# Performance work log

Measured on AMD Instinct MI355X. Metric: run time of the kernel, lower is better.

Reference implementation:

```python
import jax, jax.numpy as jnp
import numpy as np

B, D, HGT, WID = 32, 512, 8, 32   # batch, channels, feature map H, W
T = HGT * WID                     # 256 spatial tokens
NH, L, MAXLEN = 8, 2, 25          # heads, encoder layers, max text len


def _ln(x, s, b, eps=1e-5):
    m = jnp.mean(x, -1, keepdims=True)
    v = jnp.mean((x - m) ** 2, -1, keepdims=True)
    return (x - m) * jax.lax.rsqrt(v + eps) * s + b


def setup_inputs() -> dict:
    key = jax.random.key(0)
    ks = jax.random.split(key, 16)
    w = lambda k, shp: jax.random.normal(k, shp, jnp.float32) * 0.02
    return {
        "x": jax.random.normal(ks[0], (B, D, HGT, WID), jnp.float32),
        "encoder_word_pos": jnp.arange(T, dtype=jnp.int32),
        "gsrm_word_pos": jnp.arange(MAXLEN, dtype=jnp.int32),
        # encoder positional table
        "pos_table": w(ks[1], (T, D)),
        # per-layer encoder params (stacked over L)
        "ln1_s": jnp.ones((L, D), jnp.float32), "ln1_b": jnp.zeros((L, D), jnp.float32),
        "Wq": w(ks[2], (L, D, D)), "bq": jnp.zeros((L, D), jnp.float32),
        "Wk": w(ks[3], (L, D, D)), "bk": jnp.zeros((L, D), jnp.float32),
        "Wv": w(ks[4], (L, D, D)), "bv": jnp.zeros((L, D), jnp.float32),
        "Wo": w(ks[5], (L, D, D)), "bo": jnp.zeros((L, D), jnp.float32),
        "ln2_s": jnp.ones((L, D), jnp.float32), "ln2_b": jnp.zeros((L, D), jnp.float32),
        "W1": w(ks[6], (L, D, D)), "b1": jnp.zeros((L, D), jnp.float32),  # d_inner_hid = hidden_dim
        "W2": w(ks[7], (L, D, D)), "b2": jnp.zeros((L, D), jnp.float32),
        "lnf_s": jnp.ones((D,), jnp.float32), "lnf_b": jnp.zeros((D,), jnp.float32),
        # PVAM head params
        "fc0_w": w(ks[8], (D, D)), "fc0_b": jnp.zeros((D,), jnp.float32),
        "emb_table": w(ks[9], (MAXLEN, D)),
        "fc1_w": w(ks[10], (D,)),
    }


def _pvam(x, encoder_word_pos, gsrm_word_pos, pos_table,
          ln1_s, ln1_b, Wq, bq, Wk, bk, Wv, bv, Wo, bo,
          ln2_s, ln2_b, W1, b1, W2, b2, lnf_s, lnf_b,
          fc0_w, fc0_b, emb_table, fc1_w):
    b, c, h, wd = x.shape
    feat = x.reshape(b, c, h * wd).transpose(0, 2, 1)          # [b, t, c]
    # prepare encoder: scale + learned positional embedding (eval mode: no dropout)
    enc = feat * jnp.sqrt(jnp.float32(c)) + pos_table[encoder_word_pos]
    dk = c // NH
    scale = 1.0 / jnp.sqrt(jnp.float32(dk))
    for l in range(L):  # pre-norm transformer encoder (preprocess='n', postprocess='da')
        qin = _ln(enc, ln1_s[l], ln1_b[l])
        q = (qin @ Wq[l] + bq[l]).reshape(b, -1, NH, dk)
        k = (qin @ Wk[l] + bk[l]).reshape(b, -1, NH, dk)
        v = (qin @ Wv[l] + bv[l]).reshape(b, -1, NH, dk)
        p = jax.nn.softmax(jnp.einsum('bqhd,bkhd->bhqk', q, k) * scale, -1)
        o = jnp.einsum('bhqk,bkhd->bqhd', p, v).reshape(b, -1, c)
        enc = enc + (o @ Wo[l] + bo[l])
        y = _ln(enc, ln2_s[l], ln2_b[l])
        enc = enc + (jax.nn.relu(y @ W1[l] + b1[l]) @ W2[l] + b2[l])
    enc = _ln(enc, lnf_s, lnf_b)
    word_features = enc @ fc0_w + fc0_b                        # [b, t, c]
    word_pos = emb_table[gsrm_word_pos]                        # [max_len, c]
    # additive attention: tanh(broadcast add) -> scalar score -> softmax over t
    y = jnp.tanh(word_features[:, None, :, :] + word_pos[None, :, None, :])  # [b,max_len,t,c]
    attn = jax.nn.softmax(jnp.einsum('bmtc,c->bmt', y, fc1_w), -1)
    return jnp.einsum('bmt,btc->bmc', attn, word_features)    # [b, max_len, c]


def reference(x, encoder_word_pos, gsrm_word_pos, pos_table,
              ln1_s, ln1_b, Wq, bq, Wk, bk, Wv, bv, Wo, bo,
              ln2_s, ln2_b, W1, b1, W2, b2, lnf_s, lnf_b,
              fc0_w, fc0_b, emb_table, fc1_w):
    return _pvam(x, encoder_word_pos, gsrm_word_pos, pos_table,
                 ln1_s, ln1_b, Wq, bq, Wk, bk, Wv, bv, Wo, bo,
                 ln2_s, ln2_b, W1, b1, W2, b2, lnf_s, lnf_b,
                 fc0_w, fc0_b, emb_table, fc1_w)
```

## Files before the change

### kernel.cpp

```cpp
#include <hip/hip_runtime.h>
#include <math.h>

#define B_ 32
#define D_ 512
#define T_ 256
#define NH_ 8
#define DK_ 64
#define ML_ 25

typedef unsigned short ushort_t;
using short8 = __attribute__((ext_vector_type(8))) short;
using f32x4  = __attribute__((ext_vector_type(4))) float;

__device__ __forceinline__ ushort_t f2bf(float f) {
    unsigned u = __float_as_uint(f);
    unsigned r = (u + 0x7fffu + ((u >> 16) & 1u)) >> 16;
    return (ushort_t)r;
}
__device__ __forceinline__ float bf2f(ushort_t h) {
    return __uint_as_float(((unsigned)h) << 16);
}
__device__ __forceinline__ void gl16(const void* g, void* l) {
    __builtin_amdgcn_global_load_lds((const __attribute__((address_space(1))) void*)g,
                                     (__attribute__((address_space(3))) void*)l, 16, 0, 0);
}
#define ZERO4(v) { (v)[0]=0.f; (v)[1]=0.f; (v)[2]=0.f; (v)[3]=0.f; }

__global__ __launch_bounds__(256) void prep_kernel(const float* __restrict__ x,
                                                   const int* __restrict__ epos,
                                                   const float* __restrict__ pos,
                                                   float* __restrict__ enc) {
    __shared__ float ld[64][65];
    int tt = blockIdx.x, ct = blockIdx.y, b = blockIdx.z;
    int t0 = tt * 64, c0 = ct * 64;
    int tid = threadIdx.x;
    int r = tid >> 4, c4 = (tid & 15) << 2;
#pragma unroll
    for (int p = 0; p < 4; p++) {
        int row = p * 16 + r;
        float4 v = *(const float4*)(x + ((size_t)(b * D_ + c0 + row) * T_ + t0) + c4);
        ld[row][c4 + 0] = v.x; ld[row][c4 + 1] = v.y; ld[row][c4 + 2] = v.z; ld[row][c4 + 3] = v.w;
    }
    __syncthreads();
#pragma unroll
    for (int p = 0; p < 4; p++) {
        int tr = p * 16 + r;
        int ep = epos[t0 + tr];
        float4 pv = *(const float4*)(pos + (size_t)ep * D_ + c0 + c4);
        float4 o;
        o.x = ld[c4 + 0][tr] * 22.627417f + pv.x;
        o.y = ld[c4 + 1][tr] * 22.627417f + pv.y;
        o.z = ld[c4 + 2][tr] * 22.627417f + pv.z;
        o.w = ld[c4 + 3][tr] * 22.627417f + pv.w;
        *(float4*)(enc + (size_t)(b * T_ + t0 + tr) * D_ + c0 + c4) = o;
    }
}

__global__ __launch_bounds__(256) void convert_w_kernel(const float* __restrict__ Wq,
                                                        const float* __restrict__ Wk,
                                                        const float* __restrict__ Wv,
                                                        const float* __restrict__ Wo,
                                                        const float* __restrict__ W1,
                                                        const float* __restrict__ W2,
                                                        const float* __restrict__ fc0,
                                                        ushort_t* __restrict__ wt) {
    __shared__ float ld[64][65];
    int m = blockIdx.x >> 6;
    int tile = blockIdx.x & 63;
    int tn = tile >> 3, tk = tile & 7;
    int n0 = tn * 64, k0 = tk * 64;
    const float* src;
    if (m < 12) {
        int l = m / 6, w = m % 6;
        const float* bases[6] = {Wq, Wk, Wv, Wo, W1, W2};
        src = bases[w] + (size_t)l * D_ * D_;
    } else {
        src = fc0;
    }
    int tid = threadIdx.x;
    int r = tid >> 4, c4 = (tid & 15) << 2;
#pragma unroll
    for (int p = 0; p < 4; p++) {
        int row = p * 16 + r;
        float4 v = *(const float4*)(src + (size_t)(k0 + row) * D_ + n0 + c4);
        ld[row][c4 + 0] = v.x; ld[row][c4 + 1] = v.y; ld[row][c4 + 2] = v.z; ld[row][c4 + 3] = v.w;
    }
    __syncthreads();
    ushort_t* dsth = wt + (size_t)m * D_ * D_;
    ushort_t* dstl = wt + (size_t)13 * D_ * D_;
#pragma unroll
    for (int p = 0; p < 4; p++) {
        int n = p * 16 + r;
        int kc = c4;
        ushort_t h[4], lo[4];
#pragma unroll
        for (int i = 0; i < 4; i++) {
            float f = ld[kc + i][n];
            h[i] = f2bf(f);
            lo[i] = f2bf(f - bf2f(h[i]));
        }
        *(ushort4*)(dsth + (size_t)(n0 + n) * D_ + k0 + kc) = make_ushort4(h[0], h[1], h[2], h[3]);
        if (m == 12)
            *(ushort4*)(dstl + (size_t)(n0 + n) * D_ + k0 + kc) = make_ushort4(lo[0], lo[1], lo[2], lo[3]);
    }
}

template<bool LO>
__global__ __launch_bounds__(256) void ln_kernel(const float* __restrict__ x,
                                                 const float* __restrict__ s,
                                                 const float* __restrict__ b,
                                                 ushort_t* __restrict__ yh,
                                                 ushort_t* __restrict__ yl) {
    int wid = threadIdx.x >> 6, lane = threadIdx.x & 63;
    size_t row = (size_t)blockIdx.x * 4 + wid;
    const float4* xr = (const float4*)(x + row * D_);
    float4 v0 = xr[lane * 2], v1 = xr[lane * 2 + 1];
    float sum = v0.x + v0.y + v0.z + v0.w + v1.x + v1.y + v1.z + v1.w;
    for (int o = 32; o; o >>= 1) sum += __shfl_xor(sum, o);
    float mean = sum * (1.f / 512.f);
    float d[8] = {v0.x - mean, v0.y - mean, v0.z - mean, v0.w - mean,
                  v1.x - mean, v1.y - mean, v1.z - mean, v1.w - mean};
    float vs = 0.f;
#pragma unroll
    for (int i = 0; i < 8; i++) vs += d[i] * d[i];
    for (int o = 32; o; o >>= 1) vs += __shfl_xor(vs, o);
    float rs = 1.f / sqrtf(vs * (1.f / 512.f) + 1e-5f);
    const float4* s4 = (const float4*)s;
    const float4* b4 = (const float4*)b;
    float4 sa = s4[lane * 2], sb = s4[lane * 2 + 1];
    float4 ba = b4[lane * 2], bb = b4[lane * 2 + 1];
    float o8[8];
    o8[0] = d[0] * rs * sa.x + ba.x; o8[1] = d[1] * rs * sa.y + ba.y;
    o8[2] = d[2] * rs * sa.z + ba.z; o8[3] = d[3] * rs * sa.w + ba.w;
    o8[4] = d[4] * rs * sb.x + bb.x; o8[5] = d[5] * rs * sb.y + bb.y;
    o8[6] = d[6] * rs * sb.z + bb.z; o8[7] = d[7] * rs * sb.w + bb.w;
    ushort_t h[8];
#pragma unroll
    for (int i = 0; i < 8; i++) h[i] = f2bf(o8[i]);
    uint4 u;
    u.x = (unsigned)h[0] | ((unsigned)h[1] << 16);
    u.y = (unsigned)h[2] | ((unsigned)h[3] << 16);
    u.z = (unsigned)h[4] | ((unsigned)h[5] << 16);
    u.w = (unsigned)h[6] | ((unsigned)h[7] << 16);
    *(uint4*)(yh + row * D_ + lane * 8) = u;
    if (LO) {
        ushort_t l8[8];
#pragma unroll
        for (int i = 0; i < 8; i++) l8[i] = f2bf(o8[i] - bf2f(h[i]));
        uint4 ul;
        ul.x = (unsigned)l8[0] | ((unsigned)l8[1] << 16);
        ul.y = (unsigned)l8[2] | ((unsigned)l8[3] << 16);
        ul.z = (unsigned)l8[4] | ((unsigned)l8[5] << 16);
        ul.w = (unsigned)l8[6] | ((unsigned)l8[7] << 16);
        *(uint4*)(yl + row * D_ + lane * 8) = ul;
    }
}

template<int EPI>
__global__ __launch_bounds__(256) void gemm_kernel(const ushort_t* __restrict__ A0,
                                                   const ushort_t* __restrict__ A1,
                                                   const ushort_t* __restrict__ A2,
                                                   const ushort_t* __restrict__ B0,
                                                   const ushort_t* __restrict__ B1,
                                                   const ushort_t* __restrict__ B2,
                                                   int nseg, int nbn,
                                                   const float* __restrict__ bias,
                                                   const float* __restrict__ bias2,
                                                   const float* __restrict__ bias3,
                                                   const float* __restrict__ res,
                                                   float* __restrict__ outF,
                                                   ushort_t* __restrict__ outB) {
    __shared__ ushort_t As[2][128 * 64];
    __shared__ ushort_t Bs[2][128 * 64];
    int tid = threadIdx.x;
    int g = blockIdx.x;
    int per = gridDim.x >> 3;
    int lin = (g & 7) * per + (g >> 3);
    int bm = lin / nbn, bn = lin % nbn;

    int lane = tid & 63;
    int wid = tid >> 6;
    int wm = wid >> 1, wn = wid & 1;
    int xr = (lane & 7) << 3;

    f32x4 acc[4][4];
#pragma unroll
    for (int i = 0; i < 4; i++)
#pragma unroll
        for (int j = 0; j < 4; j++) ZERO4(acc[i][j]);

    int nt = nseg * 8;

#define STAGE(kt, buf)                                                                  \
    {                                                                                   \
        int seg_ = (kt) >> 3;                                                           \
        int k0_ = ((kt) & 7) * 64;                                                      \
        const ushort_t* Asg = seg_ == 0 ? A0 : (seg_ == 1 ? A1 : A2);                   \
        const ushort_t* Bsg = seg_ == 0 ? B0 : (seg_ == 1 ? B1 : B2);                   \
        _Pragma("unroll")                                                               \
        for (int it = 0; it < 4; it++) {                                                \
            int uu = tid + it * 256;                                                    \
            int row_ = uu >> 3;                                                         \
            int kb_ = (((uu & 7) ^ (row_ & 7)) << 3);                                   \
            gl16(Asg + (size_t)(bm * 128 + row_) * 512 + k0_ + kb_, &As[buf][uu * 8]);  \
            gl16(Bsg + (size_t)(bn * 128 + row_) * 512 + k0_ + kb_, &Bs[buf][uu * 8]);  \
        }                                                                               \
    }

    STAGE(0, 0);
    asm volatile("s_waitcnt vmcnt(0)" ::: "memory");
    __syncthreads();

    int buf = 0;
    for (int t = 0; t < nt; t++) {
        if (t + 1 < nt) STAGE(t + 1, buf ^ 1);
#pragma unroll
        for (int kc = 0; kc < 2; kc++) {
            short8 a[4], b[4];
            int koff = (kc * 32 + ((lane >> 4) << 3)) ^ xr;
#pragma unroll
            for (int i = 0; i < 4; i++)
                a[i] = *(const short8*)&As[buf][(wm * 64 + i * 16 + (lane & 15)) * 64 + koff];
#pragma unroll
            for (int j = 0; j < 4; j++)
                b[j] = *(const short8*)&Bs[buf][(wn * 64 + j * 16 + (lane & 15)) * 64 + koff];
#pragma unroll
            for (int i = 0; i < 4; i++)
#pragma unroll
                for (int j = 0; j < 4; j++)
                    acc[i][j] = __builtin_amdgcn_mfma_f32_16x16x32_bf16(a[i], b[j], acc[i][j], 0, 0, 0);
        }
        asm volatile("s_waitcnt vmcnt(0)" ::: "memory");
        __syncthreads();
        buf ^= 1;
    }
#undef STAGE

#pragma unroll
    for (int i = 0; i < 4; i++) {
#pragma unroll
        for (int j = 0; j < 4; j++) {
            int r0 = bm * 128 + wm * 64 + i * 16 + ((lane >> 4) << 2);
            int col = bn * 128 + wn * 64 + j * 16 + (lane & 15);
            int seg = col >> 9;
            int ccol = col & 511;
            const float* bp = bias;
            if (EPI == 5) bp = (seg == 0) ? bias : (seg == 1 ? bias2 : bias3);
            float bc = bp[EPI == 5 ? ccol : col];
#pragma unroll
            for (int jj = 0; jj < 4; jj++) {
                float v = acc[i][j][jj] + bc;
                int row = r0 + jj;
                size_t idx = (size_t)row * 512 + col;
                if (EPI == 2) {
                    outF[idx] = v + res[idx];
                } else if (EPI == 3) {
                    outB[idx] = f2bf(fmaxf(v, 0.f));
                } else if (EPI == 4) {
                    outF[idx] = v;
                } else if (EPI == 5) {
                    if (seg < 2) {
                        outB[(size_t)seg * 4194304 + (size_t)row * 512 + ccol] = f2bf(v);
                    } else {
                        int bb2 = row >> 8, t2 = row & 255;
                        outB[(size_t)2 * 4194304 +
                             ((size_t)(bb2 * 8 + (ccol >> 6)) * 64 + (ccol & 63)) * 256 + t2] = f2bf(v);
                    }
                }
            }
        }
    }
}

__global__ __launch_bounds__(256) void attn_fused_kernel(const ushort_t* __restrict__ q,
                                                         const ushort_t* __restrict__ k,
                                                         const ushort_t* __restrict__ vt,
                                                         ushort_t* __restrict__ ao) {
    __shared__ ushort_t KVs[256 * 64];
    __shared__ ushort_t Ps[64 * 256];
    int tid = threadIdx.x;
    int lane = tid & 63;
    int wid = tid >> 6;
    int m0 = blockIdx.x * 64;
    int bh = blockIdx.y;
    int b = bh >> 3, h = bh & 7;
    int xr = (lane & 7) << 3;

#pragma unroll
    for (int it = 0; it < 8; it++) {
        int uu = tid + it * 256;
        int row = uu >> 3;
        int gx = ((uu & 7) ^ (row & 7)) << 3;
        gl16(k + (size_t)(b * T_ + row) * D_ + h * DK_ + gx, &KVs[uu * 8]);
    }
    short8 qa0, qa1;
    {
        int qrow = m0 + wid * 16 + (lane & 15);
        const ushort_t* qp = q + (size_t)(b * T_ + qrow) * D_ + h * DK_ + ((lane >> 4) << 3);
        qa0 = *(const short8*)(qp);
        qa1 = *(const short8*)(qp + 32);
    }
    f32x4 acc[16];
#pragma unroll
    for (int j = 0; j < 16; j++) ZERO4(acc[j]);
    asm volatile("s_waitcnt vmcnt(0)" ::: "memory");
    __syncthreads();

#pragma unroll
    for (int j = 0; j < 16; j++) {
        int krow = j * 16 + (lane & 15);
        short8 b0 = *(const short8*)&KVs[krow * 64 + ((((lane >> 4) << 3)) ^ xr)];
        short8 b1 = *(const short8*)&KVs[krow * 64 + ((32 + ((lane >> 4) << 3)) ^ xr)];
        acc[j] = __builtin_amdgcn_mfma_f32_16x16x32_bf16(qa0, b0, acc[j], 0, 0, 0);
        acc[j] = __builtin_amdgcn_mfma_f32_16x16x32_bf16(qa1, b1, acc[j], 0, 0, 0);
    }
    __syncthreads();

#pragma unroll
    for (int it = 0; it < 8; it++) {
        int uu = tid + it * 256;
        int row = uu >> 5;
        int gx = ((uu & 31) ^ (row & 7)) << 3;
        gl16(vt + ((size_t)bh * DK_ + row) * T_ + gx, &KVs[uu * 8]);
    }

    const float C = 0.125f * 1.44269504f;
#pragma unroll
    for (int jj = 0; jj < 4; jj++) {
        float mx = -1e30f;
#pragma unroll
        for (int j = 0; j < 16; j++) mx = fmaxf(mx, acc[j][jj]);
#pragma unroll
        for (int msk = 1; msk < 16; msk <<= 1) mx = fmaxf(mx, __shfl_xor(mx, msk));
        float sm = 0.f;
#pragma unroll
        for (int j = 0; j < 16; j++) {
            float e = __builtin_amdgcn_exp2f((acc[j][jj] - mx) * C);
            acc[j][jj] = e;
            sm += e;
        }
#pragma unroll
        for (int msk = 1; msk < 16; msk <<= 1) sm += __shfl_xor(sm, msk);
        float inv = 1.f / sm;
#pragma unroll
        for (int j = 0; j < 16; j++) acc[j][jj] *= inv;
    }
#pragma unroll
    for (int j = 0; j < 16; j++) {
#pragma unroll
        for (int jj = 0; jj < 4; jj++) {
            int row = wid * 16 + ((lane >> 4) << 2) + jj;
            int col = j * 16 + (lane & 15);
            Ps[row * 256 + (col ^ ((row & 7) << 3))] = f2bf(acc[j][jj]);
        }
    }
    asm volatile("s_waitcnt vmcnt(0)" ::: "memory");
    __syncthreads();

    int wm = wid >> 1, wn = wid & 1;
    f32x4 acc2[2][2];
#pragma unroll
    for (int i = 0; i < 2; i++)
#pragma unroll
        for (int j = 0; j < 2; j++) ZERO4(acc2[i][j]);
#pragma unroll
    for (int kc = 0; kc < 8; kc++) {
        int off = (kc * 32 + ((lane >> 4) << 3)) ^ xr;
        short8 a0 = *(const short8*)&Ps[(wm * 32 + (lane & 15)) * 256 + off];
        short8 a1 = *(const short8*)&Ps[(wm * 32 + 16 + (lane & 15)) * 256 + off];
        short8 b0 = *(const short8*)&KVs[(wn * 32 + (lane & 15)) * 256 + off];
        short8 b1 = *(const short8*)&KVs[(wn * 32 + 16 + (lane & 15)) * 256 + off];
        acc2[0][0] = __builtin_amdgcn_mfma_f32_16x16x32_bf16(a0, b0, acc2[0][0], 0, 0, 0);
        acc2[0][1] = __builtin_amdgcn_mfma_f32_16x16x32_bf16(a0, b1, acc2[0][1], 0, 0, 0);
        acc2[1][0] = __builtin_amdgcn_mfma_f32_16x16x32_bf16(a1, b0, acc2[1][0], 0, 0, 0);
        acc2[1][1] = __builtin_amdgcn_mfma_f32_16x16x32_bf16(a1, b1, acc2[1][1], 0, 0, 0);
    }
#pragma unroll
    for (int i = 0; i < 2; i++)
#pragma unroll
        for (int j = 0; j < 2; j++)
#pragma unroll
            for (int jj = 0; jj < 4; jj++)
                ao[(size_t)(b * T_ + m0 + wm * 32 + i * 16 + ((lane >> 4) << 2) + jj) * D_ +
                   h * DK_ + wn * 32 + j * 16 + (lane & 15)] = f2bf(acc2[i][j][jj]);
}

__global__ __launch_bounds__(256) void scores_kernel(const float* __restrict__ wf,
                                                     const int* __restrict__ gpos,
                                                     const float* __restrict__ emb,
                                                     const float* __restrict__ w1,
                                                     float* __restrict__ scores) {
    __shared__ float wpL[5][512];
    __shared__ float w1m2[512];
    const float K2 = 2.885390082f;
    int tid = threadIdx.x;
    int b = blockIdx.y;
    int mg = blockIdx.z * 5;
    int t = blockIdx.x * 32 + (tid >> 3);
    int cg = tid & 7;
    for (int idx = tid; idx < 5 * 128; idx += 256) {
        int m = idx >> 7, w4 = idx & 127;
        float4 v = *(const float4*)(emb + (size_t)gpos[mg + m] * D_ + (w4 << 2));
        v.x *= K2; v.y *= K2; v.z *= K2; v.w *= K2;
        *(float4*)&wpL[m][w4 << 2] = v;
    }
    if (tid < 128) {
        float4 v = *(const float4*)(w1 + (tid << 2));
        v.x *= -2.f; v.y *= -2.f; v.z *= -2.f; v.w *= -2.f;
        *(float4*)&w1m2[tid << 2] = v;
    }
    float4 wfs[16];
    float W1S = 0.f;
    const float* wfr = wf + (size_t)(b * T_ + t) * D_ + (cg << 2);
#pragma unroll
    for (int j = 0; j < 16; j++) {
        float4 v = *(const float4*)(wfr + (j << 5));
        wfs[j].x = v.x * K2; wfs[j].y = v.y * K2; wfs[j].z = v.z * K2; wfs[j].w = v.w * K2;
        float4 wv = *(const float4*)(w1 + (cg << 2) + (j << 5));
        W1S += wv.x + wv.y + wv.z + wv.w;
    }
    __syncthreads();
    float s[5] = {W1S, W1S, W1S, W1S, W1S};
#pragma unroll
    for (int j = 0; j < 16; j++) {
        float4 w14 = *(const float4*)&w1m2[(cg << 2) + (j << 5)];
#pragma unroll
        for (int m = 0; m < 5; m++) {
            float4 wp4 = *(const float4*)&wpL[m][(cg << 2) + (j << 5)];
            s[m] += w14.x * __builtin_amdgcn_rcpf(__builtin_amdgcn_exp2f(wfs[j].x + wp4.x) + 1.f);
            s[m] += w14.y * __builtin_amdgcn_rcpf(__builtin_amdgcn_exp2f(wfs[j].y + wp4.y) + 1.f);
            s[m] += w14.z * __builtin_amdgcn_rcpf(__builtin_amdgcn_exp2f(wfs[j].z + wp4.z) + 1.f);
            s[m] += w14.w * __builtin_amdgcn_rcpf(__builtin_amdgcn_exp2f(wfs[j].w + wp4.w) + 1.f);
        }
    }
#pragma unroll
    for (int m = 0; m < 5; m++) {
        s[m] += __shfl_xor(s[m], 1);
        s[m] += __shfl_xor(s[m], 2);
        s[m] += __shfl_xor(s[m], 4);
    }
    if (cg == 0) {
#pragma unroll
        for (int m = 0; m < 5; m++)
            scores[((size_t)b * ML_ + mg + m) * T_ + t] = s[m];
    }
}

__global__ __launch_bounds__(256) void softmax_kernel(float* __restrict__ sc) {
    int wid = threadIdx.x >> 6, lane = threadIdx.x & 63;
    size_t row = (size_t)blockIdx.x * 4 + wid;
    float4* p = (float4*)(sc + row * T_);
    float4 v = p[lane];
    float mx = fmaxf(fmaxf(v.x, v.y), fmaxf(v.z, v.w));
    for (int o = 32; o; o >>= 1) mx = fmaxf(mx, __shfl_xor(mx, o));
    float4 e;
    e.x = __expf(v.x - mx); e.y = __expf(v.y - mx);
    e.z = __expf(v.z - mx); e.w = __expf(v.w - mx);
    float sm = e.x + e.y + e.z + e.w;
    for (int o = 32; o; o >>= 1) sm += __shfl_xor(sm, o);
    float inv = 1.f / sm;
    e.x *= inv; e.y *= inv; e.z *= inv; e.w *= inv;
    p[lane] = e;
}

__global__ __launch_bounds__(256) void wsum_kernel(const float* __restrict__ attn,
                                                   const float* __restrict__ wf,
                                                   float* __restrict__ out) {
    __shared__ float at[T_][8];
    int tid = threadIdx.x;
    int b = blockIdx.y, m0 = blockIdx.x * 5;
#pragma unroll
    for (int q = 0; q < 5; q++) {
        float a = attn[((size_t)b * ML_ + m0 + q) * T_ + tid];
        at[tid][q] = a;
    }
    __syncthreads();
    int c0 = tid << 1;
    const float* wfb = wf + (size_t)b * T_ * D_ + c0;
    float acc[5][2] = {};
    for (int t = 0; t < T_; t++) {
        float2 v = *(const float2*)(wfb + (size_t)t * D_);
        float4 a4 = *(const float4*)&at[t][0];
        float a5 = at[t][4];
        acc[0][0] += a4.x * v.x; acc[0][1] += a4.x * v.y;
        acc[1][0] += a4.y * v.x; acc[1][1] += a4.y * v.y;
        acc[2][0] += a4.z * v.x; acc[2][1] += a4.z * v.y;
        acc[3][0] += a4.w * v.x; acc[3][1] += a4.w * v.y;
        acc[4][0] += a5 * v.x;   acc[4][1] += a5 * v.y;
    }
#pragma unroll
    for (int q = 0; q < 5; q++) {
        float2 o;
        o.x = acc[q][0]; o.y = acc[q][1];
        *(float2*)(out + ((size_t)b * ML_ + m0 + q) * D_ + c0) = o;
    }
}

extern "C" void kernel_launch(void* const* d_in, const int* in_sizes, int n_in,
                              void* d_out, int out_size, void* d_ws, size_t ws_size,
                              hipStream_t stream) {
    (void)in_sizes; (void)n_in; (void)out_size; (void)ws_size;
    const float* x        = (const float*)d_in[0];
    const int*   epos     = (const int*)d_in[1];
    const int*   gpos     = (const int*)d_in[2];
    const float* pos_tab  = (const float*)d_in[3];
    const float* ln1_s    = (const float*)d_in[4];
    const float* ln1_b    = (const float*)d_in[5];
    const float* Wq       = (const float*)d_in[6];
    const float* bq       = (const float*)d_in[7];
    const float* Wk       = (const float*)d_in[8];
    const float* bk       = (const float*)d_in[9];
    const float* Wv       = (const float*)d_in[10];
    const float* bv       = (const float*)d_in[11];
    const float* Wo       = (const float*)d_in[12];
    const float* bo       = (const float*)d_in[13];
    const float* ln2_s    = (const float*)d_in[14];
    const float* ln2_b    = (const float*)d_in[15];
    const float* W1       = (const float*)d_in[16];
    const float* b1       = (const float*)d_in[17];
    const float* W2       = (const float*)d_in[18];
    const float* b2       = (const float*)d_in[19];
    const float* lnf_s    = (const float*)d_in[20];
    const float* lnf_b    = (const float*)d_in[21];
    const float* fc0_w    = (const float*)d_in[22];
    const float* fc0_b    = (const float*)d_in[23];
    const float* emb      = (const float*)d_in[24];
    const float* fc1_w    = (const float*)d_in[25];

    char* ws = (char*)d_ws;
    float*    enc = (float*)(ws);
    ushort_t* hi  = (ushort_t*)(ws + 16777216);
    ushort_t* qb  = (ushort_t*)(ws + 25165824);
    ushort_t* kb  = (ushort_t*)(ws + 33554432);
    ushort_t* lo  = (ushort_t*)(ws + 33554432);
    float*    scb = (float*)(ws + 33554432);
    ushort_t* vt  = (ushort_t*)(ws + 41943040);
    ushort_t* h1  = (ushort_t*)(ws + 41943040);
    ushort_t* ao  = (ushort_t*)(ws + 50331648);
    float*    wf  = (float*)(ws + 58720256);
    ushort_t* wt  = (ushort_t*)(ws + 75497472);
    const size_t WSL = (size_t)D_ * D_;

    convert_w_kernel<<<13 * 64, 256, 0, stream>>>(Wq, Wk, Wv, Wo, W1, W2, fc0_w, wt);
    prep_kernel<<<dim3(4, 8, 32), 256, 0, stream>>>(x, epos, pos_tab, enc);

    for (int l = 0; l < 2; l++) {
        size_t o1 = (size_t)l * D_;
        const ushort_t* WqkvT = wt + (l * 6 + 0) * WSL;
        const ushort_t* WoT = wt + (l * 6 + 3) * WSL;
        const ushort_t* W1T = wt + (l * 6 + 4) * WSL;
        const ushort_t* W2T = wt + (l * 6 + 5) * WSL;

        ln_kernel<false><<<2048, 256, 0, stream>>>(enc, ln1_s + o1, ln1_b + o1, hi, nullptr);
        gemm_kernel<5><<<768, 256, 0, stream>>>(hi, nullptr, nullptr, WqkvT, nullptr, nullptr,
                                                1, 12, bq + o1, bk + o1, bv + o1, nullptr, nullptr, qb);
        attn_fused_kernel<<<dim3(4, 256), 256, 0, stream>>>(qb, kb, vt, ao);
        gemm_kernel<2><<<256, 256, 0, stream>>>(ao, nullptr, nullptr, WoT, nullptr, nullptr,
                                                1, 4, bo + o1, nullptr, nullptr, enc, enc, nullptr);
        ln_kernel<false><<<2048, 256, 0, stream>>>(enc, ln2_s + o1, ln2_b + o1, hi, nullptr);
        gemm_kernel<3><<<256, 256, 0, stream>>>(hi, nullptr, nullptr, W1T, nullptr, nullptr,
                                                1, 4, b1 + o1, nullptr, nullptr, nullptr, nullptr, h1);
        gemm_kernel<2><<<256, 256, 0, stream>>>(h1, nullptr, nullptr, W2T, nullptr, nullptr,
                                                1, 4, b2 + o1, nullptr, nullptr, enc, enc, nullptr);
    }

    ln_kernel<true><<<2048, 256, 0, stream>>>(enc, lnf_s, lnf_b, hi, lo);
    gemm_kernel<4><<<256, 256, 0, stream>>>(hi, lo, hi, wt + 12 * WSL, wt + 12 * WSL, wt + 13 * WSL,
                                            3, 4, fc0_b, nullptr, nullptr, nullptr, wf, nullptr);
    scores_kernel<<<dim3(8, 32, 5), 256, 0, stream>>>(wf, gpos, emb, fc1_w, scb);
    softmax_kernel<<<200, 256, 0, stream>>>(scb);
    wsum_kernel<<<dim3(5, 32), 256, 0, stream>>>(scb, wf, (float*)d_out);
}
```

Baseline: 309.9 us.

## Narrow GEMM N-tile to 64 and deepen LDS pipeline to three stages

The GEMM tile shrinks from 128x128 to 128x64, which doubles the grid for every GEMM launch so more CUs are busy for these small M=8192 problems. LDS staging moves from double to triple buffering, and a partial vmcnt wait lets loads for two future k-tiles stay in flight while the current one is computed. In exchange, each block reuses its A tile less, so A traffic grows, and the MFMA work per LDS read drops.

```diff
diff --git a/kernel.cpp b/kernel.cpp
--- a/kernel.cpp
+++ b/kernel.cpp
@@ -170,8 +170,8 @@
                                                    const float* __restrict__ res,
                                                    float* __restrict__ outF,
                                                    ushort_t* __restrict__ outB) {
-    __shared__ ushort_t As[2][128 * 64];
-    __shared__ ushort_t Bs[2][128 * 64];
+    __shared__ ushort_t As[3][128 * 64];
+    __shared__ ushort_t Bs[3][64 * 64];
     int tid = threadIdx.x;
     int g = blockIdx.x;
     int per = gridDim.x >> 3;
@@ -183,11 +183,11 @@
     int wm = wid >> 1, wn = wid & 1;
     int xr = (lane & 7) << 3;
 
-    f32x4 acc[4][4];
+    f32x4 acc[4][2];
 #pragma unroll
     for (int i = 0; i < 4; i++)
 #pragma unroll
-        for (int j = 0; j < 4; j++) ZERO4(acc[i][j]);
+        for (int j = 0; j < 2; j++) ZERO4(acc[i][j]);
 
     int nt = nseg * 8;
 
@@ -203,45 +203,62 @@
             int row_ = uu >> 3;                                                         \
             int kb_ = (((uu & 7) ^ (row_ & 7)) << 3);                                   \
             gl16(Asg + (size_t)(bm * 128 + row_) * 512 + k0_ + kb_, &As[buf][uu * 8]);  \
-            gl16(Bsg + (size_t)(bn * 128 + row_) * 512 + k0_ + kb_, &Bs[buf][uu * 8]);  \
         }                                                                               \
+        _Pragma("unroll")                                                               \
+        for (int it = 0; it < 2; it++) {                                                \
+            int uu = tid + it * 256;                                                    \
+            int row_ = uu >> 3;                                                         \
+            int kb_ = (((uu & 7) ^ (row_ & 7)) << 3);                                   \
+            gl16(Bsg + (size_t)(bn * 64 + row_) * 512 + k0_ + kb_, &Bs[buf][uu * 8]);   \
+        }                                                                               \
+    }
+
+#define COMPUTE(bufc)                                                                        \
+    {                                                                                        \
+        _Pragma("unroll")                                                                    \
+        for (int kc = 0; kc < 2; kc++) {                                                     \
+            short8 a[4], b[2];                                                               \
+            int koff = (kc * 32 + ((lane >> 4) << 3)) ^ xr;                                  \
+            _Pragma("unroll")                                                                \
+            for (int i = 0; i < 4; i++)                                                      \
+                a[i] = *(const short8*)&As[bufc][(wm * 64 + i * 16 + (lane & 15)) * 64 + koff]; \
+            _Pragma("unroll")                                                                \
+            for (int j = 0; j < 2; j++)                                                      \
+                b[j] = *(const short8*)&Bs[bufc][(wn * 32 + j * 16 + (lane & 15)) * 64 + koff]; \
+            _Pragma("unroll")                                                                \
+            for (int i = 0; i < 4; i++)                                                      \
+                _Pragma("unroll")                                                            \
+                for (int j = 0; j < 2; j++)                                                  \
+                    acc[i][j] = __builtin_amdgcn_mfma_f32_16x16x32_bf16(a[i], b[j], acc[i][j], 0, 0, 0); \
+        }                                                                                    \
     }
 
     STAGE(0, 0);
-    asm volatile("s_waitcnt vmcnt(0)" ::: "memory");
-    __syncthreads();
-
-    int buf = 0;
+    if (nt > 1) STAGE(1, 1);
+    asm volatile("s_waitcnt vmcnt(6)" ::: "memory");
+    __syncthreads();
+
+    int cur = 0;
     for (int t = 0; t < nt; t++) {
-        if (t + 1 < nt) STAGE(t + 1, buf ^ 1);
-#pragma unroll
-        for (int kc = 0; kc < 2; kc++) {
-            short8 a[4], b[4];
-            int koff = (kc * 32 + ((lane >> 4) << 3)) ^ xr;
-#pragma unroll
-            for (int i = 0; i < 4; i++)
-                a[i] = *(const short8*)&As[buf][(wm * 64 + i * 16 + (lane & 15)) * 64 + koff];
-#pragma unroll
-            for (int j = 0; j < 4; j++)
-                b[j] = *(const short8*)&Bs[buf][(wn * 64 + j * 16 + (lane & 15)) * 64 + koff];
-#pragma unroll
-            for (int i = 0; i < 4; i++)
-#pragma unroll
-                for (int j = 0; j < 4; j++)
-                    acc[i][j] = __builtin_amdgcn_mfma_f32_16x16x32_bf16(a[i], b[j], acc[i][j], 0, 0, 0);
+        if (t + 2 < nt) STAGE(t + 2, (cur + 2 >= 3 ? cur - 1 : cur + 2));
+        COMPUTE(cur);
+        if (t + 2 < nt) {
+            asm volatile("s_waitcnt vmcnt(6)" ::: "memory");
+        } else if (t + 1 < nt) {
+            asm volatile("s_waitcnt vmcnt(0)" ::: "memory");
         }
-        asm volatile("s_waitcnt vmcnt(0)" ::: "memory");
         __syncthreads();
-        buf ^= 1;
+        cur = (cur == 2) ? 0 : cur + 1;
     }
 #undef STAGE
+#undef COMPUTE
 
 #pragma unroll
     for (int i = 0; i < 4; i++) {
 #pragma unroll
-        for (int j = 0; j < 4; j++) {
+        for (int j = 0; j < 2; j++) {
             int r0 = bm * 128 + wm * 64 + i * 16 + ((lane >> 4) << 2);
-            int col = bn * 128 + wn * 64 + j * 16 + (lane & 15);
+            int col = bn * 64 + wn * 32 + j * 16 + (lane & 15);
             int seg = col >> 9;
             int ccol = col & 511;
             const float* bp = bias;
@@ -552,21 +569,21 @@
         const ushort_t* W2T = wt + (l * 6 + 5) * WSL;
 
         ln_kernel<false><<<2048, 256, 0, stream>>>(enc, ln1_s + o1, ln1_b + o1, hi, nullptr);
-        gemm_kernel<5><<<768, 256, 0, stream>>>(hi, nullptr, nullptr, WqkvT, nullptr, nullptr,
-                                                1, 12, bq + o1, bk + o1, bv + o1, nullptr, nullptr, qb);
+        gemm_kernel<5><<<1536, 256, 0, stream>>>(hi, nullptr, nullptr, WqkvT, nullptr, nullptr,
+                                                 1, 24, bq + o1, bk + o1, bv + o1, nullptr, nullptr, qb);
         attn_fused_kernel<<<dim3(4, 256), 256, 0, stream>>>(qb, kb, vt, ao);
-        gemm_kernel<2><<<256, 256, 0, stream>>>(ao, nullptr, nullptr, WoT, nullptr, nullptr,
-                                                1, 4, bo + o1, nullptr, nullptr, enc, enc, nullptr);
+        gemm_kernel<2><<<512, 256, 0, stream>>>(ao, nullptr, nullptr, WoT, nullptr, nullptr,
+                                                1, 8, bo + o1, nullptr, nullptr, enc, enc, nullptr);
         ln_kernel<false><<<2048, 256, 0, stream>>>(enc, ln2_s + o1, ln2_b + o1, hi, nullptr);
-        gemm_kernel<3><<<256, 256, 0, stream>>>(hi, nullptr, nullptr, W1T, nullptr, nullptr,
-                                                1, 4, b1 + o1, nullptr, nullptr, nullptr, nullptr, h1);
-        gemm_kernel<2><<<256, 256, 0, stream>>>(h1, nullptr, nullptr, W2T, nullptr, nullptr,
-                                                1, 4, b2 + o1, nullptr, nullptr, enc, enc, nullptr);
+        gemm_kernel<3><<<512, 256, 0, stream>>>(hi, nullptr, nullptr, W1T, nullptr, nullptr,
+                                                1, 8, b1 + o1, nullptr, nullptr, nullptr, nullptr, h1);
+        gemm_kernel<2><<<512, 256, 0, stream>>>(h1, nullptr, nullptr, W2T, nullptr, nullptr,
+                                                1, 8, b2 + o1, nullptr, nullptr, enc, enc, nullptr);
     }
 
     ln_kernel<true><<<2048, 256, 0, stream>>>(enc, lnf_s, lnf_b, hi, lo);
-    gemm_kernel<4><<<256, 256, 0, stream>>>(hi, lo, hi, wt + 12 * WSL, wt + 12 * WSL, wt + 13 * WSL,
-                                            3, 4, fc0_b, nullptr, nullptr, nullptr, wf, nullptr);
+    gemm_kernel<4><<<512, 256, 0, stream>>>(hi, lo, hi, wt + 12 * WSL, wt + 12 * WSL, wt + 13 * WSL,
+                                            3, 8, fc0_b, nullptr, nullptr, nullptr, wf, nullptr);
     scores_kernel<<<dim3(8, 32, 5), 256, 0, stream>>>(wf, gpos, emb, fc1_w, scb);
     softmax_kernel<<<200, 256, 0, stream>>>(scb);
     wsum_kernel<<<dim3(5, 32), 256, 0, stream>>>(scb, wf, (float*)d_out);
```

Result: faster. 295.8 us (-4.5%).
